# Performance work log

Measured on AMD Instinct MI355X. Metric: run time of the kernel, lower is better.

Reference implementation:

```python
import jax, jax.numpy as jnp
import numpy as np
from jax import lax

B_SZ, L, D, N = 4, 2048, 768, 16


def setup_inputs() -> dict:
    key = jax.random.key(0)
    ks = jax.random.split(key, 8)
    x = jax.random.normal(ks[0], (B_SZ, L, D), dtype=jnp.float32)
    # A_log init: log(repeat(arange(1, N+1), 'n -> d n'))
    A_log = jnp.log(jnp.tile(jnp.arange(1, N + 1, dtype=jnp.float32), (D, 1)))  # (D, N)
    sD = 1.0 / np.sqrt(D)
    Wb = jax.random.normal(ks[1], (N, D), dtype=jnp.float32) * sD
    bb = jax.random.normal(ks[2], (N,), dtype=jnp.float32) * sD
    Wc = jax.random.normal(ks[3], (N, D), dtype=jnp.float32) * sD
    bc = jax.random.normal(ks[4], (N,), dtype=jnp.float32) * sD
    W1 = jax.random.normal(ks[5], (1, D), dtype=jnp.float32) * sD
    b1 = jnp.zeros((1,), dtype=jnp.float32)
    Wd = jax.random.normal(ks[6], (D, 1), dtype=jnp.float32)
    bd = jax.random.normal(ks[7], (D,), dtype=jnp.float32)
    return {"x": x, "A_log": A_log, "Wb": Wb, "bb": bb, "Wc": Wc, "bc": bc,
            "W1": W1, "b1": b1, "Wd": Wd, "bd": bd}


def reference(x, A_log, Wb, bb, Wc, bc, W1, b1, Wd, bd):
    # x: (b, l, d)
    A = -jnp.exp(A_log)                                   # (d, n)
    Bp = x @ Wb.T + bb                                    # (b, l, n)
    C = x @ Wc.T + bc                                     # (b, l, n)
    s1 = x @ W1.T + b1                                    # (b, l, 1)
    delta = jax.nn.softplus(s1 @ Wd.T + bd)               # (b, l, d)
    deltaA = jnp.exp(jnp.einsum('bld,dn->bldn', delta, A))          # (b, l, d, n)
    deltaB_u = jnp.einsum('bld,bln,bld->bldn', delta, Bp, x)        # (b, l, d, n)

    def step(h, inputs):
        dA, dBu, c = inputs                               # (b,d,n),(b,d,n),(b,n)
        h = dA * h + dBu
        y = jnp.einsum('bdn,bn->bd', h, c)
        return h, y

    b, l, d = x.shape
    n = A_log.shape[1]
    h0 = jnp.zeros((b, d, n), dtype=x.dtype)
    _, ys = lax.scan(step, h0, (jnp.moveaxis(deltaA, 1, 0),
                                jnp.moveaxis(deltaB_u, 1, 0),
                                jnp.moveaxis(C, 1, 0)))
    return jnp.moveaxis(ys, 0, 1)                          # (b, l, d)
```

## Files before the change

### kernel.cpp

```cpp
#include <hip/hip_runtime.h>
#include <math.h>

#define B_SZ 4
#define LSEQ 2048
#define DDIM 768
#define NST  16
#define NROW (B_SZ * LSEQ)
#define NJ   33

#define NC   64
#define CS   (LSEQ / NC)
#define CPG  (NC / 4)

#define KSPL 16
#define KCH  (DDIM / KSPL)

__global__ __launch_bounds__(256) void proj_part_kernel(
    const float* __restrict__ x,
    const float* __restrict__ Wb, const float* __restrict__ Wc,
    const float* __restrict__ W1, float* __restrict__ part)
{
    const int row = blockIdx.x * 256 + threadIdx.x;
    const int s = blockIdx.y;
    const int k0 = s * KCH;

    float4 xv[KCH / 4];
    const float* xp = x + (size_t)row * DDIM + k0;
    #pragma unroll
    for (int q = 0; q < KCH / 4; ++q) xv[q] = *(const float4*)(xp + q * 4);

    float acc[NJ];
    #pragma unroll
    for (int j = 0; j < NJ; ++j) {
        const float* wrow = (j < 16) ? (Wb + j * DDIM)
                          : (j < 32) ? (Wc + (j - 16) * DDIM)
                                     : W1;
        const float* wk = wrow + k0;
        float a = 0.f;
        #pragma unroll
        for (int q = 0; q < KCH / 4; ++q) {
            a = fmaf(xv[q].x, wk[q * 4 + 0], a);
            a = fmaf(xv[q].y, wk[q * 4 + 1], a);
            a = fmaf(xv[q].z, wk[q * 4 + 2], a);
            a = fmaf(xv[q].w, wk[q * 4 + 3], a);
        }
        acc[j] = a;
    }
    #pragma unroll
    for (int j = 0; j < NJ; ++j)
        part[((size_t)s * NJ + j) * NROW + row] = acc[j];
}

__global__ __launch_bounds__(256) void proj_reduce_kernel(
    const float* __restrict__ part,
    const float* __restrict__ bb, const float* __restrict__ bc,
    const float* __restrict__ b1,
    float* __restrict__ Bp, float* __restrict__ Cc, float* __restrict__ s1)
{
    const int idx = blockIdx.x * 256 + threadIdx.x;
    if (idx >= NJ * NROW) return;
    const int j = idx / NROW;
    const int row = idx % NROW;
    float a = 0.f;
    #pragma unroll
    for (int s = 0; s < KSPL; ++s)
        a += part[((size_t)s * NJ + j) * NROW + row];
    if (j < 16)      Bp[(size_t)row * NST + j] = a + bb[j];
    else if (j < 32) Cc[(size_t)row * NST + (j - 16)] = a + bc[j - 16];
    else             s1[row] = a + b1[0];
}

__device__ __forceinline__ float softplus_f(float z) {
    float t = __expf(-fabsf(z));
    return fmaxf(z, 0.f) + __logf(1.f + t);
}

__device__ __forceinline__ void powers16(float p, float* e) {
    e[0] = p;      e[1] = p * p;      e[2] = e[1] * p;   e[3] = e[1] * e[1];
    e[4] = e[3] * p;  e[5] = e[3] * e[1];  e[6] = e[3] * e[2];  e[7] = e[3] * e[3];
    e[8] = e[7] * p;  e[9] = e[7] * e[1];  e[10] = e[7] * e[2]; e[11] = e[7] * e[3];
    e[12] = e[7] * e[4]; e[13] = e[7] * e[5]; e[14] = e[7] * e[6]; e[15] = e[7] * e[7];
}

__device__ __forceinline__ bool a_structured(const float* acoef) {
    bool st = true;
    #pragma unroll
    for (int n = 0; n < NST; ++n)
        st = st && (fabsf(acoef[n] - (float)(n + 1) * acoef[0]) <= 1e-5f * fabsf(acoef[n]));
    return __all(st) != 0;
}

__global__ __launch_bounds__(256) void pass1_kernel(
    const float* __restrict__ x, const float* __restrict__ A_log,
    const float* __restrict__ Wd, const float* __restrict__ bd,
    const float* __restrict__ Bp, const float* __restrict__ s1,
    float* __restrict__ Ssum, float* __restrict__ Q)
{
    __shared__ float xs[CS][256];
    __shared__ float bs[CS][NST];
    __shared__ float ss[CS];

    const int tid = threadIdx.x;
    const int d0 = blockIdx.x * 256;
    const int d = d0 + tid;
    const int c = blockIdx.y, b = blockIdx.z;
    const int rowbase = b * LSEQ + c * CS;

    {
        const float4* xg = (const float4*)(x + (size_t)rowbase * DDIM + d0);
        #pragma unroll
        for (int i = 0; i < (CS * 256 / 4) / 256; ++i) {
            const int flat = i * 256 + tid;
            const int r = flat >> 6, q = flat & 63;
            const float4 v = xg[(size_t)r * (DDIM / 4) + q];
            float* p = &xs[r][q * 4];
            p[0] = v.x; p[1] = v.y; p[2] = v.z; p[3] = v.w;
        }
        if (tid < CS * NST / 4) {
            const float4 v = ((const float4*)(Bp + (size_t)rowbase * NST))[tid];
            const int r = tid >> 2, q = tid & 3;
            float* p = &bs[r][q * 4];
            p[0] = v.x; p[1] = v.y; p[2] = v.z; p[3] = v.w;
        }
        if (tid < CS) ss[tid] = s1[rowbase + tid];
    }

    const float wd = Wd[d], bdv = bd[d];
    float acoef[NST];
    #pragma unroll
    for (int n = 0; n < NST; ++n) acoef[n] = -__expf(A_log[d * NST + n]);
    const float a0 = acoef[0];
    const bool structured = a_structured(acoef);

    __syncthreads();

    float h[NST];
    #pragma unroll
    for (int n = 0; n < NST; ++n) h[n] = 0.f;
    float S = 0.f;

    if (structured) {
        #pragma unroll 4
        for (int l = 0; l < CS; ++l) {
            const float delta = softplus_f(fmaf(ss[l], wd, bdv));
            S += delta;
            float e[NST];
            powers16(__expf(delta * a0), e);
            const float dx = delta * xs[l][tid];
            const float4 b0 = *(const float4*)&bs[l][0];
            const float4 b1v = *(const float4*)&bs[l][4];
            const float4 b2 = *(const float4*)&bs[l][8];
            const float4 b3v = *(const float4*)&bs[l][12];
            const float bv[NST] = {b0.x, b0.y, b0.z, b0.w, b1v.x, b1v.y, b1v.z, b1v.w,
                                   b2.x, b2.y, b2.z, b2.w, b3v.x, b3v.y, b3v.z, b3v.w};
            #pragma unroll
            for (int n = 0; n < NST; ++n) h[n] = fmaf(e[n], h[n], dx * bv[n]);
        }
    } else {
        #pragma unroll 4
        for (int l = 0; l < CS; ++l) {
            const float delta = softplus_f(fmaf(ss[l], wd, bdv));
            S += delta;
            float e[NST];
            #pragma unroll
            for (int n = 0; n < NST; ++n) e[n] = __expf(delta * acoef[n]);
            const float dx = delta * xs[l][tid];
            const float4 b0 = *(const float4*)&bs[l][0];
            const float4 b1v = *(const float4*)&bs[l][4];
            const float4 b2 = *(const float4*)&bs[l][8];
            const float4 b3v = *(const float4*)&bs[l][12];
            const float bv[NST] = {b0.x, b0.y, b0.z, b0.w, b1v.x, b1v.y, b1v.z, b1v.w,
                                   b2.x, b2.y, b2.z, b2.w, b3v.x, b3v.y, b3v.z, b3v.w};
            #pragma unroll
            for (int n = 0; n < NST; ++n) h[n] = fmaf(e[n], h[n], dx * bv[n]);
        }
    }
    Ssum[((size_t)b * NC + c) * DDIM + d] = S;
    const size_t gbase = (((size_t)b * NC + c) * DDIM + d) * NST;
    float4* Q4 = (float4*)(Q + gbase);
    #pragma unroll
    for (int q = 0; q < 4; ++q)
        Q4[q] = make_float4(h[q * 4], h[q * 4 + 1], h[q * 4 + 2], h[q * 4 + 3]);
}

__global__ __launch_bounds__(256) void combine_kernel(
    const float* __restrict__ A_log,
    const float* __restrict__ Ssum, const float* __restrict__ Q,
    float* __restrict__ Hin)
{
    const int gidx = blockIdx.x * 256 + threadIdx.x;
    const int lane = threadIdx.x & 63;
    const int rlow = gidx & 15;
    const int g = (gidx >> 4) & 3;
    const int hi = gidx >> 6;
    const int pairIdx = hi * 16 + rlow;
    const int b2 = pairIdx / (DDIM * NST);
    const int r = pairIdx % (DDIM * NST);
    const int d2 = r >> 4;
    const float ac = -__expf(A_log[r]);
    const int c0 = g * CPG;

    float eq[CPG], qq[CPG];
    #pragma unroll
    for (int ci = 0; ci < CPG; ++ci) {
        const size_t base = (size_t)(b2 * NC + c0 + ci);
        eq[ci] = __expf(ac * Ssum[base * DDIM + d2]);
        qq[ci] = Q[base * (DDIM * NST) + r];
    }
    float E = 1.f, H = 0.f;
    #pragma unroll
    for (int ci = 0; ci < CPG; ++ci) { H = fmaf(eq[ci], H, qq[ci]); E *= eq[ci]; }

    float oE = __shfl_up(E, 16, 64);
    float oH = __shfl_up(H, 16, 64);
    if (lane >= 16) { H = fmaf(E, oH, H); E *= oE; }
    oE = __shfl_up(E, 32, 64);
    oH = __shfl_up(H, 32, 64);
    if (lane >= 32) { H = fmaf(E, oH, H); E *= oE; }

    float hin = __shfl_up(H, 16, 64);
    if (g == 0) hin = 0.f;

    float h = hin;
    #pragma unroll
    for (int ci = 0; ci < CPG; ++ci) {
        const size_t base = (size_t)(b2 * NC + c0 + ci);
        Hin[base * (DDIM * NST) + r] = h;
        h = fmaf(eq[ci], h, qq[ci]);
    }
}

__global__ __launch_bounds__(256) void pass2_kernel(
    const float* __restrict__ x, const float* __restrict__ A_log,
    const float* __restrict__ Wd, const float* __restrict__ bd,
    const float* __restrict__ Bp, const float* __restrict__ Cc,
    const float* __restrict__ s1, const float* __restrict__ Hin,
    float* __restrict__ out)
{
    __shared__ float xs[CS][256];
    __shared__ float bs[CS][NST];
    __shared__ float cs[CS][NST];
    __shared__ float ss[CS];

    const int tid = threadIdx.x;
    const int d0 = blockIdx.x * 256;
    const int d = d0 + tid;
    const int c = blockIdx.y, b = blockIdx.z;
    const int rowbase = b * LSEQ + c * CS;

    {
        const float4* xg = (const float4*)(x + (size_t)rowbase * DDIM + d0);
        #pragma unroll
        for (int i = 0; i < (CS * 256 / 4) / 256; ++i) {
            const int flat = i * 256 + tid;
            const int r = flat >> 6, q = flat & 63;
            const float4 v = xg[(size_t)r * (DDIM / 4) + q];
            float* p = &xs[r][q * 4];
            p[0] = v.x; p[1] = v.y; p[2] = v.z; p[3] = v.w;
        }
        if (tid < CS * NST / 4) {
            const float4 v = ((const float4*)(Bp + (size_t)rowbase * NST))[tid];
            const int r = tid >> 2, q = tid & 3;
            float* p = &bs[r][q * 4];
            p[0] = v.x; p[1] = v.y; p[2] = v.z; p[3] = v.w;
        } else {
            const int t2 = tid - 128;
            const float4 v = ((const float4*)(Cc + (size_t)rowbase * NST))[t2];
            const int r = t2 >> 2, q = t2 & 3;
            float* p = &cs[r][q * 4];
            p[0] = v.x; p[1] = v.y; p[2] = v.z; p[3] = v.w;
        }
        if (tid < CS) ss[tid] = s1[rowbase + tid];
    }

    const float wd = Wd[d], bdv = bd[d];
    float acoef[NST];
    #pragma unroll
    for (int n = 0; n < NST; ++n) acoef[n] = -__expf(A_log[d * NST + n]);
    const float a0 = acoef[0];
    const bool structured = a_structured(acoef);

    float h[NST];
    const size_t gbase = (((size_t)b * NC + c) * DDIM + d) * NST;
    const float4* H4 = (const float4*)(Hin + gbase);
    #pragma unroll
    for (int q = 0; q < 4; ++q) {
        const float4 hv = H4[q];
        h[q * 4] = hv.x; h[q * 4 + 1] = hv.y; h[q * 4 + 2] = hv.z; h[q * 4 + 3] = hv.w;
    }

    __syncthreads();

    float* yp = out + (size_t)rowbase * DDIM + d;

    if (structured) {
        #pragma unroll 4
        for (int l = 0; l < CS; ++l) {
            const float delta = softplus_f(fmaf(ss[l], wd, bdv));
            float e[NST];
            powers16(__expf(delta * a0), e);
            const float dx = delta * xs[l][tid];
            const float4 b0 = *(const float4*)&bs[l][0];
            const float4 b1v = *(const float4*)&bs[l][4];
            const float4 b2 = *(const float4*)&bs[l][8];
            const float4 b3v = *(const float4*)&bs[l][12];
            const float4 c0v = *(const float4*)&cs[l][0];
            const float4 c1v = *(const float4*)&cs[l][4];
            const float4 c2v = *(const float4*)&cs[l][8];
            const float4 c3v = *(const float4*)&cs[l][12];
            const float bv[NST] = {b0.x, b0.y, b0.z, b0.w, b1v.x, b1v.y, b1v.z, b1v.w,
                                   b2.x, b2.y, b2.z, b2.w, b3v.x, b3v.y, b3v.z, b3v.w};
            const float cv[NST] = {c0v.x, c0v.y, c0v.z, c0v.w, c1v.x, c1v.y, c1v.z, c1v.w,
                                   c2v.x, c2v.y, c2v.z, c2v.w, c3v.x, c3v.y, c3v.z, c3v.w};
            float y = 0.f;
            #pragma unroll
            for (int n = 0; n < NST; ++n) {
                h[n] = fmaf(e[n], h[n], dx * bv[n]);
                y = fmaf(h[n], cv[n], y);
            }
            yp[(size_t)l * DDIM] = y;
        }
    } else {
        #pragma unroll 4
        for (int l = 0; l < CS; ++l) {
            const float delta = softplus_f(fmaf(ss[l], wd, bdv));
            float e[NST];
            #pragma unroll
            for (int n = 0; n < NST; ++n) e[n] = __expf(delta * acoef[n]);
            const float dx = delta * xs[l][tid];
            const float4 b0 = *(const float4*)&bs[l][0];
            const float4 b1v = *(const float4*)&bs[l][4];
            const float4 b2 = *(const float4*)&bs[l][8];
            const float4 b3v = *(const float4*)&bs[l][12];
            const float4 c0v = *(const float4*)&cs[l][0];
            const float4 c1v = *(const float4*)&cs[l][4];
            const float4 c2v = *(const float4*)&cs[l][8];
            const float4 c3v = *(const float4*)&cs[l][12];
            const float bv[NST] = {b0.x, b0.y, b0.z, b0.w, b1v.x, b1v.y, b1v.z, b1v.w,
                                   b2.x, b2.y, b2.z, b2.w, b3v.x, b3v.y, b3v.z, b3v.w};
            const float cv[NST] = {c0v.x, c0v.y, c0v.z, c0v.w, c1v.x, c1v.y, c1v.z, c1v.w,
                                   c2v.x, c2v.y, c2v.z, c2v.w, c3v.x, c3v.y, c3v.z, c3v.w};
            float y = 0.f;
            #pragma unroll
            for (int n = 0; n < NST; ++n) {
                h[n] = fmaf(e[n], h[n], dx * bv[n]);
                y = fmaf(h[n], cv[n], y);
            }
            yp[(size_t)l * DDIM] = y;
        }
    }
}

extern "C" void kernel_launch(void* const* d_in, const int* in_sizes, int n_in,
                              void* d_out, int out_size, void* d_ws, size_t ws_size,
                              hipStream_t stream) {
    const float* x     = (const float*)d_in[0];
    const float* A_log = (const float*)d_in[1];
    const float* Wb    = (const float*)d_in[2];
    const float* bb    = (const float*)d_in[3];
    const float* Wc    = (const float*)d_in[4];
    const float* bc    = (const float*)d_in[5];
    const float* W1    = (const float*)d_in[6];
    const float* b1    = (const float*)d_in[7];
    const float* Wd    = (const float*)d_in[8];
    const float* bd    = (const float*)d_in[9];
    float* out = (float*)d_out;

    float* ws = (float*)d_ws;
    const size_t partN = (size_t)KSPL * NJ * NROW;
    const size_t BpN = (size_t)NROW * NST;
    const size_t s1N = (size_t)NROW;
    const size_t sN  = (size_t)B_SZ * NC * DDIM;
    const size_t agg = (size_t)B_SZ * NC * DDIM * NST;

    float* part = ws;
    float* Bp   = part + partN;
    float* Cc   = Bp + BpN;
    float* s1   = Cc + BpN;
    float* Ssum = s1 + s1N;
    float* Q    = Ssum + sN;
    float* Hin  = Q + agg;

    dim3 gproj(NROW / 256, KSPL);
    proj_part_kernel<<<gproj, 256, 0, stream>>>(x, Wb, Wc, W1, part);
    proj_reduce_kernel<<<(NJ * NROW + 255) / 256, 256, 0, stream>>>(part, bb, bc, b1, Bp, Cc, s1);

    dim3 gscan(DDIM / 256, NC, B_SZ);
    pass1_kernel<<<gscan, 256, 0, stream>>>(x, A_log, Wd, bd, Bp, s1, Ssum, Q);
    combine_kernel<<<(B_SZ * DDIM * NST * 4) / 256, 256, 0, stream>>>(A_log, Ssum, Q, Hin);
    pass2_kernel<<<gscan, 256, 0, stream>>>(x, A_log, Wd, bd, Bp, Cc, s1, Hin, out);
}
```

Baseline: 160.0 us.

## Fold chunk-carry combine into pass2 with backward early-exit accumulation

Removes the separate combine kernel and the Hin buffer. Each pass2 thread now builds its incoming state by walking earlier chunks backwards, summing each chunk's Q weighted by the accumulated decay product. The walk stops once the decay underflows to zero across the wavefront. This saves one launch and the Hin write and read, but adds a loop of up to c iterations of global Q loads per thread. The early exit depends on how fast the decay reaches zero.

After: 189.1 us. +18.2%, slower.

```diff
diff --git a/kernel.cpp b/kernel.cpp
--- a/kernel.cpp
+++ b/kernel.cpp
@@ -10,7 +10,6 @@
 
 #define NC   64
 #define CS   (LSEQ / NC)
-#define CPG  (NC / 4)
 
 #define KSPL 16
 #define KCH  (DDIM / KSPL)
@@ -183,58 +182,12 @@
         Q4[q] = make_float4(h[q * 4], h[q * 4 + 1], h[q * 4 + 2], h[q * 4 + 3]);
 }
 
-__global__ __launch_bounds__(256) void combine_kernel(
-    const float* __restrict__ A_log,
-    const float* __restrict__ Ssum, const float* __restrict__ Q,
-    float* __restrict__ Hin)
-{
-    const int gidx = blockIdx.x * 256 + threadIdx.x;
-    const int lane = threadIdx.x & 63;
-    const int rlow = gidx & 15;
-    const int g = (gidx >> 4) & 3;
-    const int hi = gidx >> 6;
-    const int pairIdx = hi * 16 + rlow;
-    const int b2 = pairIdx / (DDIM * NST);
-    const int r = pairIdx % (DDIM * NST);
-    const int d2 = r >> 4;
-    const float ac = -__expf(A_log[r]);
-    const int c0 = g * CPG;
-
-    float eq[CPG], qq[CPG];
-    #pragma unroll
-    for (int ci = 0; ci < CPG; ++ci) {
-        const size_t base = (size_t)(b2 * NC + c0 + ci);
-        eq[ci] = __expf(ac * Ssum[base * DDIM + d2]);
-        qq[ci] = Q[base * (DDIM * NST) + r];
-    }
-    float E = 1.f, H = 0.f;
-    #pragma unroll
-    for (int ci = 0; ci < CPG; ++ci) { H = fmaf(eq[ci], H, qq[ci]); E *= eq[ci]; }
-
-    float oE = __shfl_up(E, 16, 64);
-    float oH = __shfl_up(H, 16, 64);
-    if (lane >= 16) { H = fmaf(E, oH, H); E *= oE; }
-    oE = __shfl_up(E, 32, 64);
-    oH = __shfl_up(H, 32, 64);
-    if (lane >= 32) { H = fmaf(E, oH, H); E *= oE; }
-
-    float hin = __shfl_up(H, 16, 64);
-    if (g == 0) hin = 0.f;
-
-    float h = hin;
-    #pragma unroll
-    for (int ci = 0; ci < CPG; ++ci) {
-        const size_t base = (size_t)(b2 * NC + c0 + ci);
-        Hin[base * (DDIM * NST) + r] = h;
-        h = fmaf(eq[ci], h, qq[ci]);
-    }
-}
-
 __global__ __launch_bounds__(256) void pass2_kernel(
     const float* __restrict__ x, const float* __restrict__ A_log,
     const float* __restrict__ Wd, const float* __restrict__ bd,
     const float* __restrict__ Bp, const float* __restrict__ Cc,
-    const float* __restrict__ s1, const float* __restrict__ Hin,
+    const float* __restrict__ s1,
+    const float* __restrict__ Ssum, const float* __restrict__ Q,
     float* __restrict__ out)
 {
     __shared__ float xs[CS][256];
@@ -281,12 +234,55 @@
     const bool structured = a_structured(acoef);
 
     float h[NST];
-    const size_t gbase = (((size_t)b * NC + c) * DDIM + d) * NST;
-    const float4* H4 = (const float4*)(Hin + gbase);
-    #pragma unroll
-    for (int q = 0; q < 4; ++q) {
-        const float4 hv = H4[q];
-        h[q * 4] = hv.x; h[q * 4 + 1] = hv.y; h[q * 4 + 2] = hv.z; h[q * 4 + 3] = hv.w;
+    #pragma unroll
+    for (int n = 0; n < NST; ++n) h[n] = 0.f;
+
+    if (structured) {
+        float P = 1.f;
+        for (int j = c - 1; j >= 0; --j) {
+            const size_t base = (size_t)(b * NC + j);
+            float e[NST];
+            powers16(P, e);
+            if (j == c - 1) {
+                #pragma unroll
+                for (int n = 0; n < NST; ++n) e[n] = 1.f;
+            }
+            const float4* Qj = (const float4*)(Q + (base * DDIM + d) * NST);
+            #pragma unroll
+            for (int q = 0; q < 4; ++q) {
+                const float4 v = Qj[q];
+                h[q * 4 + 0] = fmaf(e[q * 4 + 0], v.x, h[q * 4 + 0]);
+                h[q * 4 + 1] = fmaf(e[q * 4 + 1], v.y, h[q * 4 + 1]);
+                h[q * 4 + 2] = fmaf(e[q * 4 + 2], v.z, h[q * 4 + 2]);
+                h[q * 4 + 3] = fmaf(e[q * 4 + 3], v.w, h[q * 4 + 3]);
+            }
+            P *= __expf(a0 * Ssum[base * DDIM + d]);
+            if (__all(P == 0.f)) break;
+        }
+    } else if (c > 0) {
+        float Pn[NST];
+        #pragma unroll
+        for (int n = 0; n < NST; ++n) Pn[n] = 1.f;
+        for (int j = c - 1; j >= 0; --j) {
+            const size_t base = (size_t)(b * NC + j);
+            const float4* Qj = (const float4*)(Q + (base * DDIM + d) * NST);
+            #pragma unroll
+            for (int q = 0; q < 4; ++q) {
+                const float4 v = Qj[q];
+                h[q * 4 + 0] = fmaf(Pn[q * 4 + 0], v.x, h[q * 4 + 0]);
+                h[q * 4 + 1] = fmaf(Pn[q * 4 + 1], v.y, h[q * 4 + 1]);
+                h[q * 4 + 2] = fmaf(Pn[q * 4 + 2], v.z, h[q * 4 + 2]);
+                h[q * 4 + 3] = fmaf(Pn[q * 4 + 3], v.w, h[q * 4 + 3]);
+            }
+            const float Sj = Ssum[base * DDIM + d];
+            float m = 0.f;
+            #pragma unroll
+            for (int n = 0; n < NST; ++n) {
+                Pn[n] *= __expf(acoef[n] * Sj);
+                m = fmaxf(m, fabsf(Pn[n]));
+            }
+            if (__all(m == 0.f)) break;
+        }
     }
 
     __syncthreads();
@@ -371,7 +367,6 @@
     const size_t BpN = (size_t)NROW * NST;
     const size_t s1N = (size_t)NROW;
     const size_t sN  = (size_t)B_SZ * NC * DDIM;
-    const size_t agg = (size_t)B_SZ * NC * DDIM * NST;
 
     float* part = ws;
     float* Bp   = part + partN;
@@ -379,7 +374,6 @@
     float* s1   = Cc + BpN;
     float* Ssum = s1 + s1N;
     float* Q    = Ssum + sN;
-    float* Hin  = Q + agg;
 
     dim3 gproj(NROW / 256, KSPL);
     proj_part_kernel<<<gproj, 256, 0, stream>>>(x, Wb, Wc, W1, part);
@@ -387,6 +381,5 @@
 
     dim3 gscan(DDIM / 256, NC, B_SZ);
     pass1_kernel<<<gscan, 256, 0, stream>>>(x, A_log, Wd, bd, Bp, s1, Ssum, Q);
-    combine_kernel<<<(B_SZ * DDIM * NST * 4) / 256, 256, 0, stream>>>(A_log, Ssum, Q, Hin);
-    pass2_kernel<<<gscan, 256, 0, stream>>>(x, A_log, Wd, bd, Bp, Cc, s1, Hin, out);
-}
+    pass2_kernel<<<gscan, 256, 0, stream>>>(x, A_log, Wd, bd, Bp, Cc, s1, Ssum, Q, out);
+}
```
